# Performance work log

Hardware: AMD Instinct MI355X
Metric: run time of the kernel (lower is better)

The kernel has to match this reference:

```python
import jax, jax.numpy as jnp
import numpy as np

N_RES = 256
D_PAIR = 128
NUM_HEADS = 16
D_HEAD = 32
D_INNER = NUM_HEADS * D_HEAD  # 512


def setup_inputs() -> dict:
    key = jax.random.key(0)
    ks = jax.random.split(key, 5)
    s_in = 1.0 / np.sqrt(D_PAIR)
    s_out = 1.0 / np.sqrt(D_INNER)
    return {
        "pair_repr": jax.random.normal(ks[0], (N_RES, N_RES, D_PAIR), jnp.float32),
        "Wq": jax.random.normal(ks[1], (D_PAIR, D_INNER), jnp.float32) * s_in,
        "bq": jnp.zeros((D_INNER,), jnp.float32),
        "Wk": jax.random.normal(ks[2], (D_PAIR, D_INNER), jnp.float32) * s_in,
        "bk": jnp.zeros((D_INNER,), jnp.float32),
        "Wv": jax.random.normal(ks[3], (D_PAIR, D_INNER), jnp.float32) * s_in,
        "bv": jnp.zeros((D_INNER,), jnp.float32),
        "Wo": jax.random.normal(ks[4], (D_INNER, D_PAIR), jnp.float32) * s_out,
        "bo": jnp.zeros((D_PAIR,), jnp.float32),
    }


def reference(pair_repr, Wq, bq, Wk, bk, Wv, bv, Wo, bo):
    N = pair_repr.shape[0]
    # Projections -> (N, N, H, Dh)
    q = (pair_repr @ Wq + bq).reshape(N, N, NUM_HEADS, D_HEAD)
    k = (pair_repr @ Wk + bk).reshape(N, N, NUM_HEADS, D_HEAD)
    v = (pair_repr @ Wv + bv).reshape(N, N, NUM_HEADS, D_HEAD)
    # Triangular attention for starting nodes: attend over k index per row i.
    a = jnp.einsum('ijhc,ikhc->ijkh', q, k) / jnp.sqrt(jnp.asarray(D_HEAD, q.dtype))
    # Lower-triangular mask over (j, k), broadcast over (i, h).
    mask = jnp.tril(jnp.ones((N, N), dtype=bool))[None, :, :, None]
    a = jnp.where(mask, a, jnp.asarray(-1e9, a.dtype))
    a = jax.nn.softmax(a, axis=2)
    o = jnp.einsum('ijkh,ikhc->ijhc', a, v).reshape(N, N, D_INNER)
    return pair_repr + (o @ Wo + bo)
```

## Files before the change

kernel.cpp:

```cpp
#include <hip/hip_runtime.h>
#include <hip/hip_bf16.h>

#define NRES 256
#define DPAIR 128
#define NHEADS 16
#define DHEAD 32
#define DINNER 512

typedef unsigned short u16;
typedef __attribute__((ext_vector_type(4))) float f32x4;
typedef __attribute__((ext_vector_type(8))) short s16x8;
typedef __attribute__((ext_vector_type(4))) short s16x4;

#define QSCALE (0.17677669529663687f * 1.4426950408889634f)

__device__ __forceinline__ u16 f32_to_bf16(float f) {
    unsigned int u = __builtin_bit_cast(unsigned int, f);
    unsigned int r = (u + 0x7FFFu + ((u >> 16) & 1u)) >> 16;
    return (u16)r;
}

__device__ __forceinline__ float fast_exp2(float x) {
#if __has_builtin(__builtin_amdgcn_exp2f)
    return __builtin_amdgcn_exp2f(x);
#else
    return exp2f(x);
#endif
}

__device__ __forceinline__ f32x4 mfma_16x16x16_bf16(s16x4 a, s16x4 b, f32x4 c) {
#if __has_builtin(__builtin_amdgcn_mfma_f32_16x16x16bf16_1k)
    return __builtin_amdgcn_mfma_f32_16x16x16bf16_1k(a, b, c, 0, 0, 0);
#elif __has_builtin(__builtin_amdgcn_mfma_f32_16x16x16_bf16)
    return __builtin_amdgcn_mfma_f32_16x16x16_bf16(a, b, c, 0, 0, 0);
#else
    f32x4 d;
    asm volatile("v_mfma_f32_16x16x16_bf16 %0, %1, %2, %3"
                 : "=v"(d) : "v"(a), "v"(b), "v"(c));
    return d;
#endif
}

__device__ __forceinline__ void gll16(const void* g, void* l) {
    __builtin_amdgcn_global_load_lds(
        (__attribute__((address_space(1))) unsigned int*)(uintptr_t)g,
        (__attribute__((address_space(3))) unsigned int*)(unsigned int)(uintptr_t)l,
        16, 0, 0);
}

__global__ __launch_bounds__(256) void prep_all(const float* __restrict__ Wq,
                                                const float* __restrict__ Wk,
                                                const float* __restrict__ Wv,
                                                const float* __restrict__ Wo,
                                                const float* __restrict__ pair,
                                                u16* wq_t, u16* wk_t, u16* wv_t, u16* wo_t,
                                                u16* __restrict__ pairb) {
    const int b = blockIdx.x;
    if (b < 1024) {
        int id = b * 256 + threadIdx.x;
        if (id < 3 * 65536) {
            int m = id / 65536;
            int e = id % 65536;
            int k = e >> 9, n = e & 511;
            const float* W = (m == 0) ? Wq : ((m == 1) ? Wk : Wv);
            u16* Wt = (m == 0) ? wq_t : ((m == 1) ? wk_t : wv_t);
            Wt[n * 128 + k] = f32_to_bf16(W[e]);
        } else {
            int e = id - 3 * 65536;
            int k = e >> 7, n = e & 127;
            wo_t[n * 512 + k] = f32_to_bf16(Wo[e]);
        }
    } else {
        const int id = (b - 1024) * 256 + threadIdx.x;
        const float4* s = reinterpret_cast<const float4*>(pair) + (size_t)id * 2;
        const float4 v0 = s[0], v1 = s[1];
        ushort4 lo, hi;
        lo.x = f32_to_bf16(v0.x); lo.y = f32_to_bf16(v0.y);
        lo.z = f32_to_bf16(v0.z); lo.w = f32_to_bf16(v0.w);
        hi.x = f32_to_bf16(v1.x); hi.y = f32_to_bf16(v1.y);
        hi.z = f32_to_bf16(v1.z); hi.w = f32_to_bf16(v1.w);
        ushort4* d = reinterpret_cast<ushort4*>(pairb + (size_t)id * 8);
        d[0] = lo; d[1] = hi;
    }
}

__global__ __launch_bounds__(512, 4) void fused_attn(const u16* __restrict__ pairb,
                                                     const u16* __restrict__ wq_t,
                                                     const u16* __restrict__ wk_t,
                                                     const u16* __restrict__ wv_t,
                                                     const float* __restrict__ bq,
                                                     const float* __restrict__ bk,
                                                     const float* __restrict__ bv,
                                                     u16* __restrict__ o_ws) {
    __shared__ __align__(128) char ldsbuf[53760];
    u16* const wS  = (u16*)ldsbuf;
    u16* const qS  = (u16*)ldsbuf;
    u16* const vTS = (u16*)(ldsbuf + 16384);
    u16* const kS  = (u16*)(ldsbuf + 33280);

    const int bx = ((blockIdx.x & 7) << 9) | (blockIdx.x >> 3);
    const int i = bx >> 4, h = bx & 15;
    const int tid = threadIdx.x;
    const int wave = tid >> 6, lane = tid & 63;
    const int g = lane >> 4, l15 = lane & 15;
    const int j0 = wave * 32;

    for (int it = 0; it < 3; ++it) {
        const int chunk = wave * 3 + it;
        const int m = chunk >> 3;
        const int lc = chunk & 7;
        const u16* Wt = (m == 0) ? wq_t : ((m == 1) ? wk_t : wv_t);
        const int c = lc * 4 + (lane >> 4);
        const int col = (lane & 15) ^ (c & 7);
        gll16((const char*)(Wt + (size_t)(h * 32) * 128) + c * 256 + col * 16,
              (void*)(wS + (m * 32 + lc * 4) * 128));
    }
    s16x8 pf[2][4];
    {
        const u16* prow = pairb + (size_t)(i * 256 + j0 + l15) * 128;
        #pragma unroll
        for (int jf = 0; jf < 2; ++jf)
            #pragma unroll
            for (int kk = 0; kk < 4; ++kk)
                pf[jf][kk] = *reinterpret_cast<const s16x8*>(prow + jf * 16 * 128 + kk * 32 + g * 8);
    }
    __syncthreads();

    f32x4 aq[2][2], ak[2][2], av[2][2];
    {
        #pragma unroll
        for (int a = 0; a < 2; ++a)
            #pragma unroll
            for (int b = 0; b < 2; ++b) {
                aq[a][b] = f32x4{0.f, 0.f, 0.f, 0.f};
                ak[a][b] = f32x4{0.f, 0.f, 0.f, 0.f};
                av[a][b] = f32x4{0.f, 0.f, 0.f, 0.f};
            }
        #pragma unroll
        for (int kk = 0; kk < 4; ++kk) {
            s16x8 wf[3][2];
            #pragma unroll
            for (int m = 0; m < 3; ++m)
                #pragma unroll
                for (int cf = 0; cf < 2; ++cf) {
                    const int c = cf * 16 + l15;
                    const int ch = (kk * 4 + g) ^ (c & 7);
                    wf[m][cf] = *reinterpret_cast<s16x8*>(&wS[(m * 32 + c) * 128 + ch * 8]);
                }
            #pragma unroll
            for (int cf = 0; cf < 2; ++cf)
                #pragma unroll
                for (int jf = 0; jf < 2; ++jf) {
                    aq[cf][jf] = __builtin_amdgcn_mfma_f32_16x16x32_bf16(wf[0][cf], pf[jf][kk], aq[cf][jf], 0, 0, 0);
                    ak[cf][jf] = __builtin_amdgcn_mfma_f32_16x16x32_bf16(wf[1][cf], pf[jf][kk], ak[cf][jf], 0, 0, 0);
                    av[jf][cf] = __builtin_amdgcn_mfma_f32_16x16x32_bf16(pf[jf][kk], wf[2][cf], av[jf][cf], 0, 0, 0);
                }
        }
    }
    __syncthreads();

    {
        #pragma unroll
        for (int cf = 0; cf < 2; ++cf) {
            const int c = cf * 16 + g * 4;
            const float4 b4q = *reinterpret_cast<const float4*>(bq + h * 32 + c);
            const float4 b4k = *reinterpret_cast<const float4*>(bk + h * 32 + c);
            #pragma unroll
            for (int jf = 0; jf < 2; ++jf) {
                const int j = j0 + jf * 16 + l15;
                ushort4 oq, ok;
                oq.x = f32_to_bf16((aq[cf][jf][0] + b4q.x) * QSCALE);
                oq.y = f32_to_bf16((aq[cf][jf][1] + b4q.y) * QSCALE);
                oq.z = f32_to_bf16((aq[cf][jf][2] + b4q.z) * QSCALE);
                oq.w = f32_to_bf16((aq[cf][jf][3] + b4q.w) * QSCALE);
                *reinterpret_cast<ushort4*>(
                    &qS[j * 32 + (((cf << 1) + (g >> 1)) ^ (j & 3)) * 8 + (g & 1) * 4]) = oq;
                ok.x = f32_to_bf16(ak[cf][jf][0] + b4k.x);
                ok.y = f32_to_bf16(ak[cf][jf][1] + b4k.y);
                ok.z = f32_to_bf16(ak[cf][jf][2] + b4k.z);
                ok.w = f32_to_bf16(ak[cf][jf][3] + b4k.w);
                *reinterpret_cast<ushort4*>(&kS[j * 40 + c]) = ok;
            }
        }
        #pragma unroll
        for (int cf = 0; cf < 2; ++cf) {
            const int c = cf * 16 + l15;
            const float bvv = bv[h * 32 + c];
            #pragma unroll
            for (int jf = 0; jf < 2; ++jf) {
                const int j = j0 + jf * 16 + g * 4;
                ushort4 ov;
                ov.x = f32_to_bf16(av[jf][cf][0] + bvv);
                ov.y = f32_to_bf16(av[jf][cf][1] + bvv);
                ov.z = f32_to_bf16(av[jf][cf][2] + bvv);
                ov.w = f32_to_bf16(av[jf][cf][3] + bvv);
                *reinterpret_cast<ushort4*>(&vTS[c * 264 + j]) = ov;
            }
        }
    }
    __syncthreads();

    const size_t obase = ((size_t)i * 256) * 512 + h * 32;
    const int tA = wave, tB = 15 - wave;

    const s16x8 qfA = *reinterpret_cast<const s16x8*>(
        &qS[(tA * 16 + l15) * 32 + (g ^ (l15 & 3)) * 8]);
    const s16x8 qfB = *reinterpret_cast<const s16x8*>(
        &qS[(tB * 16 + l15) * 32 + (g ^ (l15 & 3)) * 8]);

    f32x4 accA0 = {0.f, 0.f, 0.f, 0.f}, accA1 = {0.f, 0.f, 0.f, 0.f};
    f32x4 accB0 = {0.f, 0.f, 0.f, 0.f}, accB1 = {0.f, 0.f, 0.f, 0.f};
    float sumA = 0.f, sumB = 0.f;

    auto rdK = [&](int kt) {
        return *reinterpret_cast<s16x8*>(&kS[(kt * 16 + l15) * 40 + g * 8]);
    };
    auto rdV0 = [&](int kt) {
        return *reinterpret_cast<s16x4*>(&vTS[l15 * 264 + kt * 16 + g * 4]);
    };
    auto rdV1 = [&](int kt) {
        return *reinterpret_cast<s16x4*>(&vTS[(16 + l15) * 264 + kt * 16 + g * 4]);
    };
    auto tile = [&](const s16x8& kf, const s16x4& va0, const s16x4& va1,
                    const s16x8& qf, f32x4& a0, f32x4& a1, float& sm, bool dg) {
        f32x4 s = __builtin_amdgcn_mfma_f32_16x16x32_bf16(kf, qf, f32x4{0.f, 0.f, 0.f, 0.f}, 0, 0, 0);
        float p0, p1, p2, p3;
        if (dg) {
            p0 = ((g * 4 + 0) > l15) ? 0.f : fast_exp2(s[0]);
            p1 = ((g * 4 + 1) > l15) ? 0.f : fast_exp2(s[1]);
            p2 = ((g * 4 + 2) > l15) ? 0.f : fast_exp2(s[2]);
            p3 = ((g * 4 + 3) > l15) ? 0.f : fast_exp2(s[3]);
        } else {
            p0 = fast_exp2(s[0]); p1 = fast_exp2(s[1]);
            p2 = fast_exp2(s[2]); p3 = fast_exp2(s[3]);
        }
        sm += (p0 + p1) + (p2 + p3);
        unsigned e0 = __builtin_bit_cast(unsigned, p0) + 0x8000u;
        unsigned e1 = __builtin_bit_cast(unsigned, p1) + 0x8000u;
        unsigned e2 = __builtin_bit_cast(unsigned, p2) + 0x8000u;
        unsigned e3 = __builtin_bit_cast(unsigned, p3) + 0x8000u;
        uint2 pw;
        pw.x = __builtin_amdgcn_perm(e1, e0, 0x07060302u);
        pw.y = __builtin_amdgcn_perm(e3, e2, 0x07060302u);
        const s16x4 pb = __builtin_bit_cast(s16x4, pw);
        a0 = mfma_16x16x16_bf16(va0, pb, a0);
        a1 = mfma_16x16x16_bf16(va1, pb, a1);
    };

    for (int kt = 0; kt < tA; ++kt) {
        const s16x8 kf = rdK(kt);
        const s16x4 v0 = rdV0(kt), v1 = rdV1(kt);
        tile(kf, v0, v1, qfB, accB0, accB1, sumB, false);
        tile(kf, v0, v1, qfA, accA0, accA1, sumA, false);
    }
    {
        const s16x8 kf = rdK(tA);
        const s16x4 v0 = rdV0(tA), v1 = rdV1(tA);
        tile(kf, v0, v1, qfB, accB0, accB1, sumB, false);
        tile(kf, v0, v1, qfA, accA0, accA1, sumA, true);
    }
    for (int kt = tA + 1; kt < tB; ++kt) {
        const s16x8 kf = rdK(kt);
        const s16x4 v0 = rdV0(kt), v1 = rdV1(kt);
        tile(kf, v0, v1, qfB, accB0, accB1, sumB, false);
    }
    {
        const s16x8 kf = rdK(tB);
        const s16x4 v0 = rdV0(tB), v1 = rdV1(tB);
        tile(kf, v0, v1, qfB, accB0, accB1, sumB, true);
    }

    auto store_o = [&](int jbase, const f32x4& o0, const f32x4& o1, float sum) {
        sum += __shfl_xor(sum, 16, 64);
        sum += __shfl_xor(sum, 32, 64);
        const float rinv = 1.0f / sum;
        unsigned x0 = __builtin_bit_cast(unsigned, o0[0] * rinv) + 0x8000u;
        unsigned x1 = __builtin_bit_cast(unsigned, o0[1] * rinv) + 0x8000u;
        unsigned x2 = __builtin_bit_cast(unsigned, o0[2] * rinv) + 0x8000u;
        unsigned x3 = __builtin_bit_cast(unsigned, o0[3] * rinv) + 0x8000u;
        uint2 w0;
        w0.x = __builtin_amdgcn_perm(x1, x0, 0x07060302u);
        w0.y = __builtin_amdgcn_perm(x3, x2, 0x07060302u);
        unsigned y0 = __builtin_bit_cast(unsigned, o1[0] * rinv) + 0x8000u;
        unsigned y1 = __builtin_bit_cast(unsigned, o1[1] * rinv) + 0x8000u;
        unsigned y2 = __builtin_bit_cast(unsigned, o1[2] * rinv) + 0x8000u;
        unsigned y3 = __builtin_bit_cast(unsigned, o1[3] * rinv) + 0x8000u;
        uint2 w1;
        w1.x = __builtin_amdgcn_perm(y1, y0, 0x07060302u);
        w1.y = __builtin_amdgcn_perm(y3, y2, 0x07060302u);
        u16* orow = o_ws + obase + (size_t)(jbase + l15) * 512;
        *reinterpret_cast<uint2*>(orow + g * 4) = w0;
        *reinterpret_cast<uint2*>(orow + 16 + g * 4) = w1;
    };
    store_o(tA * 16, accA0, accA1, sumA);
    store_o(tB * 16, accB0, accB1, sumB);
}

__global__ __launch_bounds__(256) void outproj(const u16* __restrict__ o_ws,
                                               const u16* __restrict__ wo_t,
                                               const float* __restrict__ pair,
                                               const float* __restrict__ bo,
                                               float* __restrict__ out) {
    __shared__ u16 As[64 * 72];
    __shared__ u16 Bs[128 * 72];
    const int tid = threadIdx.x;
    const int m0 = blockIdx.x * 64;
    const int wave = tid >> 6, lane = tid & 63;
    const int g = lane >> 4, l15 = lane & 15;

    f32x4 acc[8];
    for (int c = 0; c < 8; ++c) acc[c] = f32x4{0.f, 0.f, 0.f, 0.f};

    for (int kt = 0; kt < 8; ++kt) {
        __syncthreads();
        for (int it = 0; it < 2; ++it) {
            int L = tid + it * 256;
            int row = L >> 3, seg = L & 7;
            *reinterpret_cast<s16x8*>(&As[row * 72 + seg * 8]) =
                *reinterpret_cast<const s16x8*>(o_ws + (size_t)(m0 + row) * 512 + kt * 64 + seg * 8);
        }
        for (int it = 0; it < 4; ++it) {
            int L = tid + it * 256;
            int n = L >> 3, seg = L & 7;
            *reinterpret_cast<s16x8*>(&Bs[n * 72 + seg * 8]) =
                *reinterpret_cast<const s16x8*>(wo_t + (size_t)n * 512 + kt * 64 + seg * 8);
        }
        __syncthreads();
        for (int kk = 0; kk < 2; ++kk) {
            const s16x8 a = *reinterpret_cast<s16x8*>(&As[(wave * 16 + l15) * 72 + kk * 32 + g * 8]);
            for (int c = 0; c < 8; ++c) {
                const s16x8 b = *reinterpret_cast<s16x8*>(&Bs[(c * 16 + l15) * 72 + kk * 32 + g * 8]);
                acc[c] = __builtin_amdgcn_mfma_f32_16x16x32_bf16(a, b, acc[c], 0, 0, 0);
            }
        }
    }

    for (int c = 0; c < 8; ++c) {
        const int n = c * 16 + l15;
        const float bias = bo[n];
        for (int r = 0; r < 4; ++r) {
            const size_t row = m0 + wave * 16 + g * 4 + r;
            out[row * 128 + n] = acc[c][r] + bias + pair[row * 128 + n];
        }
    }
}

extern "C" void kernel_launch(void* const* d_in, const int* in_sizes, int n_in,
                              void* d_out, int out_size, void* d_ws, size_t ws_size,
                              hipStream_t stream) {
    const float* pair = (const float*)d_in[0];
    const float* Wq = (const float*)d_in[1];
    const float* bq = (const float*)d_in[2];
    const float* Wk = (const float*)d_in[3];
    const float* bk = (const float*)d_in[4];
    const float* Wv = (const float*)d_in[5];
    const float* bv = (const float*)d_in[6];
    const float* Wo = (const float*)d_in[7];
    const float* bo = (const float*)d_in[8];
    float* out = (float*)d_out;

    char* ws = (char*)d_ws;
    u16* o_ws  = (u16*)(ws);
    u16* wq_t  = (u16*)(ws + 67108864);
    u16* wk_t  = wq_t + 65536;
    u16* wv_t  = wk_t + 65536;
    u16* wo_t  = wv_t + 65536;
    u16* pairb = (u16*)(ws + 67108864 + 1048576);

    prep_all<<<5120, 256, 0, stream>>>(Wq, Wk, Wv, Wo, pair,
                                       wq_t, wk_t, wv_t, wo_t, pairb);
    fused_attn<<<4096, 512, 0, stream>>>(pairb, wq_t, wk_t, wv_t, bq, bk, bv, o_ws);
    outproj<<<1024, 256, 0, stream>>>(o_ws, wo_t, pair, bo, out);
}
```

Before: 115.4 us.

## Compute softmax row sums via MFMA with ones, add setprio and block swizzle

Replaces the per-lane scalar accumulation of softmax denominators and the cross-lane shuffles with an extra MFMA against a vector of bf16 ones, so the sum comes out in the accumulator layout. Wraps the attention loop in s_setprio to favour waves issuing MFMAs, factors bf16 packing into a helper, and remaps outproj block indices so neighbouring blocks are spread across XCDs. The extra MFMA per tile adds matrix work and sums bf16-rounded probabilities, while removing VALU adds and shuffles.

```diff
diff --git a/kernel.cpp b/kernel.cpp
--- a/kernel.cpp
+++ b/kernel.cpp
@@ -18,6 +18,12 @@
     unsigned int u = __builtin_bit_cast(unsigned int, f);
     unsigned int r = (u + 0x7FFFu + ((u >> 16) & 1u)) >> 16;
     return (u16)r;
+}
+
+__device__ __forceinline__ unsigned pk2(float a, float b) {
+    unsigned ua = __builtin_bit_cast(unsigned, a) + 0x8000u;
+    unsigned ub = __builtin_bit_cast(unsigned, b) + 0x8000u;
+    return __builtin_amdgcn_perm(ub, ua, 0x07060302u);
 }
 
 __device__ __forceinline__ float fast_exp2(float x) {
@@ -168,18 +174,14 @@
             #pragma unroll
             for (int jf = 0; jf < 2; ++jf) {
                 const int j = j0 + jf * 16 + l15;
-                ushort4 oq, ok;
-                oq.x = f32_to_bf16((aq[cf][jf][0] + b4q.x) * QSCALE);
-                oq.y = f32_to_bf16((aq[cf][jf][1] + b4q.y) * QSCALE);
-                oq.z = f32_to_bf16((aq[cf][jf][2] + b4q.z) * QSCALE);
-                oq.w = f32_to_bf16((aq[cf][jf][3] + b4q.w) * QSCALE);
-                *reinterpret_cast<ushort4*>(
+                uint2 oq, ok;
+                oq.x = pk2((aq[cf][jf][0] + b4q.x) * QSCALE, (aq[cf][jf][1] + b4q.y) * QSCALE);
+                oq.y = pk2((aq[cf][jf][2] + b4q.z) * QSCALE, (aq[cf][jf][3] + b4q.w) * QSCALE);
+                *reinterpret_cast<uint2*>(
                     &qS[j * 32 + (((cf << 1) + (g >> 1)) ^ (j & 3)) * 8 + (g & 1) * 4]) = oq;
-                ok.x = f32_to_bf16(ak[cf][jf][0] + b4k.x);
-                ok.y = f32_to_bf16(ak[cf][jf][1] + b4k.y);
-                ok.z = f32_to_bf16(ak[cf][jf][2] + b4k.z);
-                ok.w = f32_to_bf16(ak[cf][jf][3] + b4k.w);
-                *reinterpret_cast<ushort4*>(&kS[j * 40 + c]) = ok;
+                ok.x = pk2(ak[cf][jf][0] + b4k.x, ak[cf][jf][1] + b4k.y);
+                ok.y = pk2(ak[cf][jf][2] + b4k.z, ak[cf][jf][3] + b4k.w);
+                *reinterpret_cast<uint2*>(&kS[j * 40 + c]) = ok;
             }
         }
         #pragma unroll
@@ -189,12 +191,10 @@
             #pragma unroll
             for (int jf = 0; jf < 2; ++jf) {
                 const int j = j0 + jf * 16 + g * 4;
-                ushort4 ov;
-                ov.x = f32_to_bf16(av[jf][cf][0] + bvv);
-                ov.y = f32_to_bf16(av[jf][cf][1] + bvv);
-                ov.z = f32_to_bf16(av[jf][cf][2] + bvv);
-                ov.w = f32_to_bf16(av[jf][cf][3] + bvv);
-                *reinterpret_cast<ushort4*>(&vTS[c * 264 + j]) = ov;
+                uint2 ov;
+                ov.x = pk2(av[jf][cf][0] + bvv, av[jf][cf][1] + bvv);
+                ov.y = pk2(av[jf][cf][2] + bvv, av[jf][cf][3] + bvv);
+                *reinterpret_cast<uint2*>(&vTS[c * 264 + j]) = ov;
             }
         }
     }
@@ -208,9 +208,10 @@
     const s16x8 qfB = *reinterpret_cast<const s16x8*>(
         &qS[(tB * 16 + l15) * 32 + (g ^ (l15 & 3)) * 8]);
 
-    f32x4 accA0 = {0.f, 0.f, 0.f, 0.f}, accA1 = {0.f, 0.f, 0.f, 0.f};
-    f32x4 accB0 = {0.f, 0.f, 0.f, 0.f}, accB1 = {0.f, 0.f, 0.f, 0.f};
-    float sumA = 0.f, sumB = 0.f;
+    const s16x4 vone = {(short)0x3F80, (short)0x3F80, (short)0x3F80, (short)0x3F80};
+
+    f32x4 accA0 = {0.f, 0.f, 0.f, 0.f}, accA1 = {0.f, 0.f, 0.f, 0.f}, accA2 = {0.f, 0.f, 0.f, 0.f};
+    f32x4 accB0 = {0.f, 0.f, 0.f, 0.f}, accB1 = {0.f, 0.f, 0.f, 0.f}, accB2 = {0.f, 0.f, 0.f, 0.f};
 
     auto rdK = [&](int kt) {
         return *reinterpret_cast<s16x8*>(&kS[(kt * 16 + l15) * 40 + g * 8]);
@@ -222,7 +223,7 @@
         return *reinterpret_cast<s16x4*>(&vTS[(16 + l15) * 264 + kt * 16 + g * 4]);
     };
     auto tile = [&](const s16x8& kf, const s16x4& va0, const s16x4& va1,
-                    const s16x8& qf, f32x4& a0, f32x4& a1, float& sm, bool dg) {
+                    const s16x8& qf, f32x4& a0, f32x4& a1, f32x4& a2, bool dg) {
         f32x4 s = __builtin_amdgcn_mfma_f32_16x16x32_bf16(kf, qf, f32x4{0.f, 0.f, 0.f, 0.f}, 0, 0, 0);
         float p0, p1, p2, p3;
         if (dg) {
@@ -234,66 +235,53 @@
             p0 = fast_exp2(s[0]); p1 = fast_exp2(s[1]);
             p2 = fast_exp2(s[2]); p3 = fast_exp2(s[3]);
         }
-        sm += (p0 + p1) + (p2 + p3);
-        unsigned e0 = __builtin_bit_cast(unsigned, p0) + 0x8000u;
-        unsigned e1 = __builtin_bit_cast(unsigned, p1) + 0x8000u;
-        unsigned e2 = __builtin_bit_cast(unsigned, p2) + 0x8000u;
-        unsigned e3 = __builtin_bit_cast(unsigned, p3) + 0x8000u;
         uint2 pw;
-        pw.x = __builtin_amdgcn_perm(e1, e0, 0x07060302u);
-        pw.y = __builtin_amdgcn_perm(e3, e2, 0x07060302u);
+        pw.x = pk2(p0, p1);
+        pw.y = pk2(p2, p3);
         const s16x4 pb = __builtin_bit_cast(s16x4, pw);
         a0 = mfma_16x16x16_bf16(va0, pb, a0);
         a1 = mfma_16x16x16_bf16(va1, pb, a1);
-    };
-
+        a2 = mfma_16x16x16_bf16(vone, pb, a2);
+    };
+
+    __builtin_amdgcn_s_setprio(1);
     for (int kt = 0; kt < tA; ++kt) {
         const s16x8 kf = rdK(kt);
         const s16x4 v0 = rdV0(kt), v1 = rdV1(kt);
-        tile(kf, v0, v1, qfB, accB0, accB1, sumB, false);
-        tile(kf, v0, v1, qfA, accA0, accA1, sumA, false);
+        tile(kf, v0, v1, qfB, accB0, accB1, accB2, false);
+        tile(kf, v0, v1, qfA, accA0, accA1, accA2, false);
     }
     {
         const s16x8 kf = rdK(tA);
         const s16x4 v0 = rdV0(tA), v1 = rdV1(tA);
-        tile(kf, v0, v1, qfB, accB0, accB1, sumB, false);
-        tile(kf, v0, v1, qfA, accA0, accA1, sumA, true);
+        tile(kf, v0, v1, qfB, accB0, accB1, accB2, false);
+        tile(kf, v0, v1, qfA, accA0, accA1, accA2, true);
     }
     for (int kt = tA + 1; kt < tB; ++kt) {
         const s16x8 kf = rdK(kt);
         const s16x4 v0 = rdV0(kt), v1 = rdV1(kt);
-        tile(kf, v0, v1, qfB, accB0, accB1, sumB, false);
+        tile(kf, v0, v1, qfB, accB0, accB1, accB2, false);
     }
     {
         const s16x8 kf = rdK(tB);
         const s16x4 v0 = rdV0(tB), v1 = rdV1(tB);
-        tile(kf, v0, v1, qfB, accB0, accB1, sumB, true);
-    }
+        tile(kf, v0, v1, qfB, accB0, accB1, accB2, true);
+    }
+    __builtin_amdgcn_s_setprio(0);
 
     auto store_o = [&](int jbase, const f32x4& o0, const f32x4& o1, float sum) {
-        sum += __shfl_xor(sum, 16, 64);
-        sum += __shfl_xor(sum, 32, 64);
         const float rinv = 1.0f / sum;
-        unsigned x0 = __builtin_bit_cast(unsigned, o0[0] * rinv) + 0x8000u;
-        unsigned x1 = __builtin_bit_cast(unsigned, o0[1] * rinv) + 0x8000u;
-        unsigned x2 = __builtin_bit_cast(unsigned, o0[2] * rinv) + 0x8000u;
-        unsigned x3 = __builtin_bit_cast(unsigned, o0[3] * rinv) + 0x8000u;
-        uint2 w0;
-        w0.x = __builtin_amdgcn_perm(x1, x0, 0x07060302u);
-        w0.y = __builtin_amdgcn_perm(x3, x2, 0x07060302u);
-        unsigned y0 = __builtin_bit_cast(unsigned, o1[0] * rinv) + 0x8000u;
-        unsigned y1 = __builtin_bit_cast(unsigned, o1[1] * rinv) + 0x8000u;
-        unsigned y2 = __builtin_bit_cast(unsigned, o1[2] * rinv) + 0x8000u;
-        unsigned y3 = __builtin_bit_cast(unsigned, o1[3] * rinv) + 0x8000u;
-        uint2 w1;
-        w1.x = __builtin_amdgcn_perm(y1, y0, 0x07060302u);
-        w1.y = __builtin_amdgcn_perm(y3, y2, 0x07060302u);
+        uint2 w0, w1;
+        w0.x = pk2(o0[0] * rinv, o0[1] * rinv);
+        w0.y = pk2(o0[2] * rinv, o0[3] * rinv);
+        w1.x = pk2(o1[0] * rinv, o1[1] * rinv);
+        w1.y = pk2(o1[2] * rinv, o1[3] * rinv);
         u16* orow = o_ws + obase + (size_t)(jbase + l15) * 512;
         *reinterpret_cast<uint2*>(orow + g * 4) = w0;
         *reinterpret_cast<uint2*>(orow + 16 + g * 4) = w1;
     };
-    store_o(tA * 16, accA0, accA1, sumA);
-    store_o(tB * 16, accB0, accB1, sumB);
+    store_o(tA * 16, accA0, accA1, accA2[0]);
+    store_o(tB * 16, accB0, accB1, accB2[0]);
 }
 
 __global__ __launch_bounds__(256) void outproj(const u16* __restrict__ o_ws,
@@ -304,7 +292,9 @@
     __shared__ u16 As[64 * 72];
     __shared__ u16 Bs[128 * 72];
     const int tid = threadIdx.x;
-    const int m0 = blockIdx.x * 64;
+    const int d = blockIdx.x;
+    const int bb = ((d & 7) << 7) | (d >> 3);
+    const int m0 = bb * 64;
     const int wave = tid >> 6, lane = tid & 63;
     const int g = lane >> 4, l15 = lane & 15;
 
```

New measurement: 114.9 us. Within noise of the previous version (-0.5%).
